# Optimization experiments

Hardware: AMD Instinct MI355X
Metric: run time of the kernel (lower is better)

Reference implementation:

```python
import jax, jax.numpy as jnp
import numpy as np

EPS = 1e-5  # torch LayerNorm default
B, P, E, H = 16, 2048, 768, 256


def setup_inputs() -> dict:
    key = jax.random.key(0)
    k_x, k_qkv, k_lw = jax.random.split(key, 3)
    return {
        "x": jax.random.normal(k_x, (B, P, E), dtype=jnp.float32),
        "norm_w": jnp.ones((P, E), dtype=jnp.float32),
        "norm_b": jnp.zeros((P, E), dtype=jnp.float32),
        "qkv_w": jax.random.normal(k_qkv, (E, 3 * H), dtype=jnp.float32) * 0.02,
        "lin_w": jax.random.normal(k_lw, (E, H), dtype=jnp.float32) * 0.02,
        "lin_b": jnp.zeros((E,), dtype=jnp.float32),
    }


def reference(x, norm_w, norm_b, qkv_w, lin_w, lin_b):
    # LayerNorm over the last TWO dims (P, E) jointly, per batch element
    mean = jnp.mean(x, axis=(1, 2), keepdims=True)
    var = jnp.var(x, axis=(1, 2), keepdims=True)
    xn = (x - mean) * jax.lax.rsqrt(var + EPS) * norm_w + norm_b

    # QKV projection: [B,P,E] @ [E,3H] -> [B,P,3H]
    qkv = jnp.einsum("bpe,eh->bph", xn, qkv_w)
    q, k, v = jnp.split(qkv, 3, axis=2)  # each [B,P,H]

    # Unnormalized attention (no scale, no softmax)
    atten = jnp.einsum("bpd,bqd->bpq", q, k)  # [B,P,P]
    o = jnp.einsum("bpq,bqd->bpd", atten, v)  # [B,P,H]

    # Dropout p=0.0 (eval) -> identity; then Linear(H -> E) + ReLU
    out = jnp.einsum("bph,eh->bpe", o, lin_w) + lin_b
    return jax.nn.relu(out)
```

## Files before the change

kernel.cpp:

```cpp
#include <hip/hip_runtime.h>
#include <cstdint>

typedef unsigned short u16;
typedef __bf16 bf16x8 __attribute__((ext_vector_type(8)));
typedef float floatx4 __attribute__((ext_vector_type(4)));

#define BB 16
#define PP 2048
#define EE 768
#define HH 256
#define PE (PP * EE)
#define MM (BB * PP)

__device__ __forceinline__ u16 f2bf(float f) {
  union { float f; uint32_t u; } v; v.f = f;
  return (u16)((v.u + 0x7fffu + ((v.u >> 16) & 1u)) >> 16);
}

__device__ __forceinline__ void gload16(const void* g, void* l) {
  typedef __attribute__((address_space(1))) const void GV;
  typedef __attribute__((address_space(3))) void LV;
  __builtin_amdgcn_global_load_lds((GV*)g, (LV*)l, 16, 0, 0);
}

__device__ __forceinline__ int xcd_remap(int orig, int nwg) {
  return (orig & 7) * (nwg >> 3) + (orig >> 3);
}

__device__ __forceinline__ void zero_acc(floatx4 acc[4][4]) {
  const floatx4 z = {0.f, 0.f, 0.f, 0.f};
#pragma unroll
  for (int i = 0; i < 4; ++i)
#pragma unroll
    for (int j = 0; j < 4; ++j) acc[i][j] = z;
}

__device__ __forceinline__ void gemm_core(const u16* A, int lda, const u16* B, int ldb,
                                          int kIters, u16* As, u16* Bs,
                                          floatx4 acc[4][4]) {
  const int tid  = threadIdx.x;
  const int lane = tid & 63;
  const int wr   = (tid >> 7) & 1;
  const int wc   = (tid >> 6) & 1;
  const int srow = tid >> 3;
  const int scol = (tid & 7) << 3;
  const int mrow = lane & 15;
  const int kgrp = (lane >> 4) << 3;
  for (int kk = 0; kk < kIters; ++kk) {
    const u16* Ak = A + kk * 64;
    const u16* Bk = B + kk * 64;
    __syncthreads();
#pragma unroll
    for (int r = 0; r < 4; ++r) {
      gload16(Ak + (size_t)(r * 32 + srow) * lda + scol, (char*)As + r * 4096 + tid * 16);
      gload16(Bk + (size_t)(r * 32 + srow) * ldb + scol, (char*)Bs + r * 4096 + tid * 16);
    }
    __syncthreads();
#pragma unroll
    for (int kp = 0; kp < 2; ++kp) {
      const int ko = kp * 32 + kgrp;
      bf16x8 af[4], bq[4];
#pragma unroll
      for (int i = 0; i < 4; ++i) {
        af[i] = *(const bf16x8*)(As + (wr * 64 + i * 16 + mrow) * 64 + ko);
        bq[i] = *(const bf16x8*)(Bs + (wc * 64 + i * 16 + mrow) * 64 + ko);
      }
#pragma unroll
      for (int i = 0; i < 4; ++i)
#pragma unroll
        for (int j = 0; j < 4; ++j)
          acc[i][j] = __builtin_amdgcn_mfma_f32_16x16x32_bf16(af[i], bq[j], acc[i][j], 0, 0, 0);
    }
  }
}

template <typename F>
__device__ __forceinline__ void epilogue(floatx4 acc[4][4], F f) {
  const int lane = threadIdx.x & 63;
  const int wr = (threadIdx.x >> 7) & 1, wc = (threadIdx.x >> 6) & 1;
  const int r0 = (lane >> 4) * 4, c0 = lane & 15;
#pragma unroll
  for (int i = 0; i < 4; ++i)
#pragma unroll
    for (int j = 0; j < 4; ++j)
#pragma unroll
      for (int r = 0; r < 4; ++r)
        f(wr * 64 + i * 16 + r0 + r, wc * 64 + j * 16 + c0, acc[i][j][r]);
}

__global__ __launch_bounds__(256) void k_reduce1(const float* __restrict__ x,
                                                 float* __restrict__ psum,
                                                 float* __restrict__ psq) {
  const int b = blockIdx.y, blk = blockIdx.x, tid = threadIdx.x;
  const float4* xb = (const float4*)(x + (size_t)b * PE + (size_t)blk * 12288);
  float s = 0.f, q = 0.f;
#pragma unroll
  for (int i = 0; i < 12; ++i) {
    float4 v = xb[tid + i * 256];
    s += v.x + v.y + v.z + v.w;
    q += v.x * v.x + v.y * v.y + v.z * v.z + v.w * v.w;
  }
  for (int off = 32; off > 0; off >>= 1) { s += __shfl_down(s, off); q += __shfl_down(q, off); }
  __shared__ float ls[4], lq[4];
  if ((tid & 63) == 0) { ls[tid >> 6] = s; lq[tid >> 6] = q; }
  __syncthreads();
  if (tid == 0) {
    psum[b * 128 + blk] = ls[0] + ls[1] + ls[2] + ls[3];
    psq [b * 128 + blk] = lq[0] + lq[1] + lq[2] + lq[3];
  }
}

__global__ void k_reduce2(const float* __restrict__ psum, const float* __restrict__ psq,
                          float* __restrict__ stats) {
  const int b = blockIdx.x, tid = threadIdx.x;
  float s = psum[b * 128 + tid], q = psq[b * 128 + tid];
  for (int off = 32; off > 0; off >>= 1) { s += __shfl_down(s, off); q += __shfl_down(q, off); }
  __shared__ float ls[2], lq[2];
  if ((tid & 63) == 0) { ls[tid >> 6] = s; lq[tid >> 6] = q; }
  __syncthreads();
  if (tid == 0) {
    float S = ls[0] + ls[1], Q = lq[0] + lq[1];
    const float invN = 1.f / (float)PE;
    float mean = S * invN;
    float var = Q * invN - mean * mean;
    stats[b * 2] = mean;
    stats[b * 2 + 1] = rsqrtf(var + 1e-5f);
  }
}

__global__ __launch_bounds__(256) void k_ln(const float* __restrict__ x,
                                            const float* __restrict__ w,
                                            const float* __restrict__ bia,
                                            const float* __restrict__ stats,
                                            u16* __restrict__ xn) {
  const float4* x4 = (const float4*)x;
  const float4* w4 = (const float4*)w;
  const float4* b4 = (const float4*)bia;
  for (int vi = blockIdx.x * 256 + threadIdx.x; vi < (PE / 4) * BB; vi += gridDim.x * 256) {
    int bidx = vi / (PE / 4);
    int wi = vi - bidx * (PE / 4);
    float4 xv = x4[vi], wv = w4[wi], bv = b4[wi];
    float mean = stats[bidx * 2], rstd = stats[bidx * 2 + 1];
    ushort4 o;
    o.x = f2bf((xv.x - mean) * rstd * wv.x + bv.x);
    o.y = f2bf((xv.y - mean) * rstd * wv.y + bv.y);
    o.z = f2bf((xv.z - mean) * rstd * wv.z + bv.z);
    o.w = f2bf((xv.w - mean) * rstd * wv.w + bv.w);
    ((ushort4*)xn)[vi] = o;
  }
}

__global__ void k_transpose_w(const float* __restrict__ src, u16* __restrict__ dst) {
  __shared__ float t[32][33];
  const int e0 = blockIdx.x * 32, n0 = blockIdx.y * 32;
  const int tx = threadIdx.x, ty = threadIdx.y;
#pragma unroll
  for (int j = 0; j < 4; ++j)
    t[ty + j * 8][tx] = src[(size_t)(e0 + ty + j * 8) * 768 + n0 + tx];
  __syncthreads();
#pragma unroll
  for (int j = 0; j < 4; ++j)
    dst[(size_t)(n0 + ty + j * 8) * 768 + e0 + tx] = f2bf(t[tx][ty + j * 8]);
}

__global__ void k_cast(const float* __restrict__ src, u16* __restrict__ dst, int n4) {
  int i = blockIdx.x * 256 + threadIdx.x;
  if (i < n4) {
    float4 v = ((const float4*)src)[i];
    ushort4 o;
    o.x = f2bf(v.x); o.y = f2bf(v.y); o.z = f2bf(v.z); o.w = f2bf(v.w);
    ((ushort4*)dst)[i] = o;
  }
}

__global__ __launch_bounds__(256) void k_gemm_qkv(const u16* __restrict__ xn,
                                                  const u16* __restrict__ wT,
                                                  u16* __restrict__ q_buf,
                                                  u16* __restrict__ kT,
                                                  u16* __restrict__ vT) {
  __shared__ __align__(16) u16 sbuf[128 * 64 * 2];
  u16* As = sbuf;
  u16* Bs = sbuf + 128 * 64;
  floatx4 acc[4][4];
  zero_acc(acc);
  const int t = xcd_remap(blockIdx.x, 1536);
  const int xt = t % 6, yt = t / 6;
  const int tM = yt * 128, tN = xt * 128;
  gemm_core(xn + (size_t)tM * EE, EE, wT + (size_t)tN * EE, EE, 12, As, Bs, acc);

  if (xt < 2) {
    epilogue(acc, [&](int gr, int gc, float v) {
      q_buf[(size_t)(tM + gr) * HH + xt * 128 + gc] = f2bf(v);
    });
  } else {
    const int b = yt >> 4;
    const int p_base = (yt & 15) * 128;
    u16* dst = ((xt < 4) ? kT : vT) + (size_t)b * (HH * PP);
    const int dbase = (xt - ((xt < 4) ? 2 : 4)) * 128;
    u16 (*tt)[144] = (u16(*)[144])sbuf;
    const int tid = threadIdx.x;
    const int lane = tid & 63;
    const int wr = (tid >> 7) & 1, wc = (tid >> 6) & 1;
    const int r0 = (lane >> 4) * 4, c0 = lane & 15;
#pragma unroll
    for (int h = 0; h < 2; ++h) {
      __syncthreads();
      if (wc == h) {
#pragma unroll
        for (int i = 0; i < 4; ++i)
#pragma unroll
          for (int j = 0; j < 4; ++j)
#pragma unroll
            for (int r = 0; r < 4; ++r)
              tt[j * 16 + c0][wr * 64 + i * 16 + r0 + r] = f2bf(acc[i][j][r]);
      }
      __syncthreads();
#pragma unroll
      for (int pass = 0; pass < 4; ++pass) {
        const int row = pass * 16 + (tid >> 4);
        const int p8 = (tid & 15) * 8;
        const int d = dbase + h * 64 + row;
        uint4 vdat = *(const uint4*)&tt[row][p8];
        *(uint4*)&dst[(size_t)d * PP + p_base + p8] = vdat;
      }
    }
  }
}

__global__ __launch_bounds__(256) void k_gemm_w2(const u16* __restrict__ kT,
                                                 const u16* __restrict__ vT,
                                                 float* __restrict__ part) {
  __shared__ __align__(16) u16 As[128 * 64], Bs[128 * 64];
  floatx4 acc[4][4];
  zero_acc(acc);
  const int t = xcd_remap(blockIdx.x, 512);
  const int xt = t & 1, yt = (t >> 1) & 1, z = t >> 2;
  const int b = z >> 3, s = z & 7;
  const int tM = yt * 128, tN = xt * 128;
  const u16* A = kT + (size_t)b * (HH * PP) + (size_t)tM * PP + s * 256;
  const u16* B = vT + (size_t)b * (HH * PP) + (size_t)tN * PP + s * 256;
  gemm_core(A, PP, B, PP, 4, As, Bs, acc);
  float* P = part + (size_t)z * 65536;
  epilogue(acc, [&](int gr, int gc, float v) {
    P[(size_t)(tM + gr) * 256 + tN + gc] = v;
  });
}

__global__ void k_reduce_w2(const float* __restrict__ part, u16* __restrict__ W2) {
  const int idx = blockIdx.x * 256 + threadIdx.x;
  const int b = idx >> 16, i = idx & 65535;
  const float* p = part + ((size_t)b << 19) + i;
  float s = 0.f;
#pragma unroll
  for (int t = 0; t < 8; ++t) s += p[(size_t)t << 16];
  W2[idx] = f2bf(s);
}

__global__ __launch_bounds__(256) void k_gemm_m2(const u16* __restrict__ lwB,
                                                 const u16* __restrict__ W2,
                                                 u16* __restrict__ M2T) {
  __shared__ __align__(16) u16 As[128 * 64], Bs[128 * 64];
  floatx4 acc[4][4];
  zero_acc(acc);
  const int t = xcd_remap(blockIdx.x, 192);
  const int xt = t & 1, yt = (t >> 1) % 6, b = t / 12;
  const int tM = yt * 128, tN = xt * 128;
  const u16* A = lwB + (size_t)tM * HH;
  const u16* B = W2 + (size_t)b * 65536 + (size_t)tN * HH;
  gemm_core(A, HH, B, HH, 4, As, Bs, acc);
  u16* Mb = M2T + (size_t)b * (EE * HH);
  epilogue(acc, [&](int gr, int gc, float v) {
    Mb[(size_t)(tM + gr) * HH + tN + gc] = f2bf(v);
  });
}

__global__ __launch_bounds__(256) void k_gemm_out(const u16* __restrict__ q_buf,
                                                  const u16* __restrict__ M2T,
                                                  const float* __restrict__ lb,
                                                  float* __restrict__ out) {
  __shared__ __align__(16) u16 As[128 * 64], Bs[128 * 64];
  floatx4 acc[4][4];
  zero_acc(acc);
  const int t = xcd_remap(blockIdx.x, 1536);
  const int xt = t % 6, yt = (t / 6) % 16, b = t / 96;
  const int tM = yt * 128, tN = xt * 128;
  const u16* A = q_buf + (size_t)b * (PP * HH) + (size_t)tM * HH;
  const u16* B = M2T + (size_t)b * (EE * HH) + (size_t)tN * HH;
  gemm_core(A, HH, B, HH, 4, As, Bs, acc);
  float* ob = out + (size_t)b * PE;
  epilogue(acc, [&](int gr, int gc, float v) {
    ob[(size_t)(tM + gr) * EE + tN + gc] = fmaxf(v + lb[tN + gc], 0.f);
  });
}

extern "C" void kernel_launch(void* const* d_in, const int* in_sizes, int n_in,
                              void* d_out, int out_size, void* d_ws, size_t ws_size,
                              hipStream_t stream) {
  (void)in_sizes; (void)n_in; (void)out_size;
  const float* x  = (const float*)d_in[0];
  const float* nw = (const float*)d_in[1];
  const float* nb = (const float*)d_in[2];
  const float* qw = (const float*)d_in[3];
  const float* lw = (const float*)d_in[4];
  const float* lb = (const float*)d_in[5];
  float* out = (float*)d_out;
  char* ws = (char*)d_ws;

  size_t off = 0;
  auto alloc = [&](size_t bytes) { size_t o = off; off += (bytes + 255) & ~(size_t)255; return o; };
  const size_t o_psum = alloc(16 * 128 * 4);
  const size_t o_psq  = alloc(16 * 128 * 4);
  const size_t o_st   = alloc(16 * 2 * 4);
  const size_t o_qwT  = alloc((size_t)768 * 768 * 2);
  const size_t o_lwB  = alloc((size_t)768 * 256 * 2);
  const size_t o_q    = alloc((size_t)MM * HH * 2);
  const size_t o_kT   = alloc((size_t)BB * HH * PP * 2);
  const size_t o_vT   = alloc((size_t)BB * HH * PP * 2);
  const size_t o_W2   = alloc((size_t)BB * HH * HH * 2);
  const size_t o_M2T  = alloc((size_t)BB * EE * HH * 2);
  const size_t need_base = off;
  const size_t region = (size_t)MM * EE * 2;

  char* big = (ws_size >= need_base + region) ? (ws + need_base) : (char*)d_out;

  float* psum = (float*)(ws + o_psum);
  float* psq  = (float*)(ws + o_psq);
  float* st   = (float*)(ws + o_st);
  u16* qwT    = (u16*)(ws + o_qwT);
  u16* lwB    = (u16*)(ws + o_lwB);
  u16* q_buf  = (u16*)(ws + o_q);
  u16* kT     = (u16*)(ws + o_kT);
  u16* vT     = (u16*)(ws + o_vT);
  u16* W2     = (u16*)(ws + o_W2);
  u16* M2T    = (u16*)(ws + o_M2T);
  u16* xn     = (u16*)big;
  float* part = (float*)big;

  k_reduce1<<<dim3(128, 16), 256, 0, stream>>>(x, psum, psq);
  k_reduce2<<<16, 128, 0, stream>>>(psum, psq, st);
  k_ln<<<2048, 256, 0, stream>>>(x, nw, nb, st, xn);
  k_transpose_w<<<dim3(24, 24), dim3(32, 8), 0, stream>>>(qw, qwT);
  k_cast<<<192, 256, 0, stream>>>(lw, lwB, 768 * 256 / 4);
  k_gemm_qkv<<<1536, 256, 0, stream>>>(xn, qwT, q_buf, kT, vT);
  k_gemm_w2<<<512, 256, 0, stream>>>(kT, vT, part);
  k_reduce_w2<<<4096, 256, 0, stream>>>(part, W2);
  k_gemm_m2<<<192, 256, 0, stream>>>(lwB, W2, M2T);
  k_gemm_out<<<1536, 256, 0, stream>>>(q_buf, M2T, lb, out);
}
```

Measured before the change: 329.7 us.

## Rewrite QKV GEMM as 256x256-tile 8-wave kernel with swizzled double-buffered LDS

Replaces the 128x128-tile QKV projection GEMM with a 256x256-tile kernel using 512 threads (8 waves), an XOR-swizzled LDS layout and double-buffered global-to-LDS loads that overlap with MFMA phases. It also adds wave priority hints. Larger tiles raise operand reuse and reduce global traffic, and the pipelining is meant to hide load latency. In exchange it uses 128KB of LDS and more accumulator registers per thread, which limits occupancy, and it launches only 384 blocks, which may leave the GPU's compute units less evenly loaded.

```diff
diff --git a/kernel.cpp b/kernel.cpp
--- a/kernel.cpp
+++ b/kernel.cpp
@@ -27,7 +27,7 @@
   return (orig & 7) * (nwg >> 3) + (orig >> 3);
 }
 
-__device__ __forceinline__ void zero_acc(floatx4 acc[4][4]) {
+__device__ __forceinline__ void zero_acc4(floatx4 acc[4][4]) {
   const floatx4 z = {0.f, 0.f, 0.f, 0.f};
 #pragma unroll
   for (int i = 0; i < 4; ++i)
@@ -75,7 +75,7 @@
 }
 
 template <typename F>
-__device__ __forceinline__ void epilogue(floatx4 acc[4][4], F f) {
+__device__ __forceinline__ void epilogue4(floatx4 acc[4][4], F f) {
   const int lane = threadIdx.x & 63;
   const int wr = (threadIdx.x >> 7) & 1, wc = (threadIdx.x >> 6) & 1;
   const int r0 = (lane >> 4) * 4, c0 = lane & 15;
@@ -86,6 +86,151 @@
 #pragma unroll
       for (int r = 0; r < 4; ++r)
         f(wr * 64 + i * 16 + r0 + r, wc * 64 + j * 16 + c0, acc[i][j][r]);
+}
+
+
+__device__ __forceinline__ void stage8(u16* sm, int bf, const u16* A, const u16* Bw,
+                                       int ks, int tid) {
+  const int colc = (((tid & 7) ^ ((tid >> 3) & 7)) << 3) + ks * 64;
+  const int rw = tid >> 3;
+#pragma unroll
+  for (int h = 0; h < 2; ++h)
+#pragma unroll
+    for (int L = 0; L < 2; ++L)
+      gload16(A + (size_t)(h * 128 + L * 64 + rw) * EE + colc,
+              (char*)sm + (size_t)(bf * 16384 + h * 8192 + L * 4096 + tid * 8) * 2);
+#pragma unroll
+  for (int h = 0; h < 2; ++h)
+#pragma unroll
+    for (int L = 0; L < 2; ++L)
+      gload16(Bw + (size_t)(h * 128 + L * 64 + rw) * EE + colc,
+              (char*)sm + (size_t)(32768 + bf * 16384 + h * 8192 + L * 4096 + tid * 8) * 2);
+}
+
+template <int IH, int JH>
+__device__ __forceinline__ void phase_mfma(const u16* sm, int bf, int wr, int wcn,
+                                           int lane, floatx4 acc[8][4]) {
+  const int m = lane & 15, hi = lane >> 4, mk = m & 7;
+  bf16x8 a[4][2], b[2][2];
+#pragma unroll
+  for (int ii = 0; ii < 4; ++ii) {
+    const int r = (IH * 4 + ii) * 16 + m;
+#pragma unroll
+    for (int kp = 0; kp < 2; ++kp)
+      a[ii][kp] = *(const bf16x8*)(sm + bf * 16384 + wr * 8192 + r * 64 +
+                                   (((kp * 4 + hi) ^ mk) << 3));
+  }
+#pragma unroll
+  for (int jj = 0; jj < 2; ++jj) {
+    const int r = (wcn & 1) * 64 + (JH * 2 + jj) * 16 + m;
+#pragma unroll
+    for (int kp = 0; kp < 2; ++kp)
+      b[jj][kp] = *(const bf16x8*)(sm + 32768 + bf * 16384 + (wcn >> 1) * 8192 + r * 64 +
+                                   (((kp * 4 + hi) ^ mk) << 3));
+  }
+  __builtin_amdgcn_s_barrier();
+  __builtin_amdgcn_s_setprio(1);
+#pragma unroll
+  for (int ii = 0; ii < 4; ++ii)
+#pragma unroll
+    for (int jj = 0; jj < 2; ++jj)
+#pragma unroll
+      for (int kp = 0; kp < 2; ++kp)
+        acc[IH * 4 + ii][JH * 2 + jj] = __builtin_amdgcn_mfma_f32_16x16x32_bf16(
+            a[ii][kp], b[jj][kp], acc[IH * 4 + ii][JH * 2 + jj], 0, 0, 0);
+  __builtin_amdgcn_s_setprio(0);
+}
+
+__global__ __launch_bounds__(512, 2) void k_gemm_qkv8(const u16* __restrict__ xn,
+                                                      const u16* __restrict__ wT,
+                                                      u16* __restrict__ q_buf,
+                                                      u16* __restrict__ kT,
+                                                      u16* __restrict__ vT) {
+  __shared__ __align__(16) u16 sm[65536];
+  floatx4 acc[8][4];
+  const floatx4 z = {0.f, 0.f, 0.f, 0.f};
+#pragma unroll
+  for (int i = 0; i < 8; ++i)
+#pragma unroll
+    for (int j = 0; j < 4; ++j) acc[i][j] = z;
+
+  const int t = xcd_remap(blockIdx.x, 384);
+  const int xt = t % 3;
+  const int yt = t / 3;
+  const int tM = yt * 256, tN = xt * 256;
+  const u16* A  = xn + (size_t)tM * EE;
+  const u16* Bw = wT + (size_t)tN * EE;
+  const int tid = threadIdx.x, lane = tid & 63, wid = tid >> 6;
+  const int wr = wid >> 2, wcn = wid & 3;
+
+  stage8(sm, 0, A, Bw, 0, tid);
+  asm volatile("s_waitcnt vmcnt(0)" ::: "memory");
+  __builtin_amdgcn_sched_barrier(0);
+  __builtin_amdgcn_s_barrier();
+
+  const int NT2 = (EE / 64) / 2;
+  for (int it = 0; it < NT2; ++it) {
+    stage8(sm, 1, A, Bw, 2 * it + 1, tid);
+    phase_mfma<0, 0>(sm, 0, wr, wcn, lane, acc);
+    __builtin_amdgcn_s_barrier();
+    phase_mfma<0, 1>(sm, 0, wr, wcn, lane, acc);
+    __builtin_amdgcn_s_barrier();
+    phase_mfma<1, 0>(sm, 0, wr, wcn, lane, acc);
+    __builtin_amdgcn_s_barrier();
+    phase_mfma<1, 1>(sm, 0, wr, wcn, lane, acc);
+    asm volatile("s_waitcnt vmcnt(0)" ::: "memory");
+    __builtin_amdgcn_sched_barrier(0);
+    __builtin_amdgcn_s_barrier();
+    if (2 * it + 2 < EE / 64) stage8(sm, 0, A, Bw, 2 * it + 2, tid);
+    phase_mfma<0, 0>(sm, 1, wr, wcn, lane, acc);
+    __builtin_amdgcn_s_barrier();
+    phase_mfma<0, 1>(sm, 1, wr, wcn, lane, acc);
+    __builtin_amdgcn_s_barrier();
+    phase_mfma<1, 0>(sm, 1, wr, wcn, lane, acc);
+    __builtin_amdgcn_s_barrier();
+    phase_mfma<1, 1>(sm, 1, wr, wcn, lane, acc);
+    asm volatile("s_waitcnt vmcnt(0)" ::: "memory");
+    __builtin_amdgcn_sched_barrier(0);
+    __builtin_amdgcn_s_barrier();
+  }
+
+  const int c0 = lane & 15, r0v = (lane >> 4) * 4;
+  if (xt == 0) {
+#pragma unroll
+    for (int i = 0; i < 8; ++i)
+#pragma unroll
+      for (int j = 0; j < 4; ++j)
+#pragma unroll
+        for (int r = 0; r < 4; ++r)
+          q_buf[(size_t)(tM + wr * 128 + i * 16 + r0v + r) * HH + wcn * 64 + j * 16 + c0] =
+              f2bf(acc[i][j][r]);
+  } else {
+    u16* dst = (xt == 1 ? kT : vT);
+    const int b = yt >> 3, p0 = (yt & 7) * 256;
+    u16* db = dst + (size_t)b * (HH * PP);
+    u16* tt = sm + wid * 8192;
+#pragma unroll
+    for (int jh = 0; jh < 2; ++jh) {
+#pragma unroll
+      for (int jj = 0; jj < 2; ++jj)
+#pragma unroll
+        for (int i = 0; i < 8; ++i) {
+          ushort4 w4;
+          w4.x = f2bf(acc[i][jh * 2 + jj][0]);
+          w4.y = f2bf(acc[i][jh * 2 + jj][1]);
+          w4.z = f2bf(acc[i][jh * 2 + jj][2]);
+          w4.w = f2bf(acc[i][jh * 2 + jj][3]);
+          *(ushort4*)&tt[(jj * 16 + c0) * 136 + i * 16 + r0v] = w4;
+        }
+#pragma unroll
+      for (int pass = 0; pass < 8; ++pass) {
+        const int dl = pass * 4 + (lane >> 4), p8 = (lane & 15) * 8;
+        uint4 vdat = *(const uint4*)&tt[dl * 136 + p8];
+        const int d = wcn * 64 + jh * 32 + dl;
+        *(uint4*)&db[(size_t)d * PP + p0 + wr * 128 + p8] = vdat;
+      }
+    }
+  }
 }
 
 __global__ __launch_bounds__(256) void k_reduce1(const float* __restrict__ x,
@@ -173,66 +318,12 @@
   }
 }
 
-__global__ __launch_bounds__(256) void k_gemm_qkv(const u16* __restrict__ xn,
-                                                  const u16* __restrict__ wT,
-                                                  u16* __restrict__ q_buf,
-                                                  u16* __restrict__ kT,
-                                                  u16* __restrict__ vT) {
-  __shared__ __align__(16) u16 sbuf[128 * 64 * 2];
-  u16* As = sbuf;
-  u16* Bs = sbuf + 128 * 64;
-  floatx4 acc[4][4];
-  zero_acc(acc);
-  const int t = xcd_remap(blockIdx.x, 1536);
-  const int xt = t % 6, yt = t / 6;
-  const int tM = yt * 128, tN = xt * 128;
-  gemm_core(xn + (size_t)tM * EE, EE, wT + (size_t)tN * EE, EE, 12, As, Bs, acc);
-
-  if (xt < 2) {
-    epilogue(acc, [&](int gr, int gc, float v) {
-      q_buf[(size_t)(tM + gr) * HH + xt * 128 + gc] = f2bf(v);
-    });
-  } else {
-    const int b = yt >> 4;
-    const int p_base = (yt & 15) * 128;
-    u16* dst = ((xt < 4) ? kT : vT) + (size_t)b * (HH * PP);
-    const int dbase = (xt - ((xt < 4) ? 2 : 4)) * 128;
-    u16 (*tt)[144] = (u16(*)[144])sbuf;
-    const int tid = threadIdx.x;
-    const int lane = tid & 63;
-    const int wr = (tid >> 7) & 1, wc = (tid >> 6) & 1;
-    const int r0 = (lane >> 4) * 4, c0 = lane & 15;
-#pragma unroll
-    for (int h = 0; h < 2; ++h) {
-      __syncthreads();
-      if (wc == h) {
-#pragma unroll
-        for (int i = 0; i < 4; ++i)
-#pragma unroll
-          for (int j = 0; j < 4; ++j)
-#pragma unroll
-            for (int r = 0; r < 4; ++r)
-              tt[j * 16 + c0][wr * 64 + i * 16 + r0 + r] = f2bf(acc[i][j][r]);
-      }
-      __syncthreads();
-#pragma unroll
-      for (int pass = 0; pass < 4; ++pass) {
-        const int row = pass * 16 + (tid >> 4);
-        const int p8 = (tid & 15) * 8;
-        const int d = dbase + h * 64 + row;
-        uint4 vdat = *(const uint4*)&tt[row][p8];
-        *(uint4*)&dst[(size_t)d * PP + p_base + p8] = vdat;
-      }
-    }
-  }
-}
-
 __global__ __launch_bounds__(256) void k_gemm_w2(const u16* __restrict__ kT,
                                                  const u16* __restrict__ vT,
                                                  float* __restrict__ part) {
   __shared__ __align__(16) u16 As[128 * 64], Bs[128 * 64];
   floatx4 acc[4][4];
-  zero_acc(acc);
+  zero_acc4(acc);
   const int t = xcd_remap(blockIdx.x, 512);
   const int xt = t & 1, yt = (t >> 1) & 1, z = t >> 2;
   const int b = z >> 3, s = z & 7;
@@ -241,7 +332,7 @@
   const u16* B = vT + (size_t)b * (HH * PP) + (size_t)tN * PP + s * 256;
   gemm_core(A, PP, B, PP, 4, As, Bs, acc);
   float* P = part + (size_t)z * 65536;
-  epilogue(acc, [&](int gr, int gc, float v) {
+  epilogue4(acc, [&](int gr, int gc, float v) {
     P[(size_t)(tM + gr) * 256 + tN + gc] = v;
   });
 }
@@ -261,7 +352,7 @@
                                                  u16* __restrict__ M2T) {
   __shared__ __align__(16) u16 As[128 * 64], Bs[128 * 64];
   floatx4 acc[4][4];
-  zero_acc(acc);
+  zero_acc4(acc);
   const int t = xcd_remap(blockIdx.x, 192);
   const int xt = t & 1, yt = (t >> 1) % 6, b = t / 12;
   const int tM = yt * 128, tN = xt * 128;
@@ -269,7 +360,7 @@
   const u16* B = W2 + (size_t)b * 65536 + (size_t)tN * HH;
   gemm_core(A, HH, B, HH, 4, As, Bs, acc);
   u16* Mb = M2T + (size_t)b * (EE * HH);
-  epilogue(acc, [&](int gr, int gc, float v) {
+  epilogue4(acc, [&](int gr, int gc, float v) {
     Mb[(size_t)(tM + gr) * HH + tN + gc] = f2bf(v);
   });
 }
@@ -280,7 +371,7 @@
                                                   float* __restrict__ out) {
   __shared__ __align__(16) u16 As[128 * 64], Bs[128 * 64];
   floatx4 acc[4][4];
-  zero_acc(acc);
+  zero_acc4(acc);
   const int t = xcd_remap(blockIdx.x, 1536);
   const int xt = t % 6, yt = (t / 6) % 16, b = t / 96;
   const int tM = yt * 128, tN = xt * 128;
@@ -288,7 +379,7 @@
   const u16* B = M2T + (size_t)b * (EE * HH) + (size_t)tN * HH;
   gemm_core(A, HH, B, HH, 4, As, Bs, acc);
   float* ob = out + (size_t)b * PE;
-  epilogue(acc, [&](int gr, int gc, float v) {
+  epilogue4(acc, [&](int gr, int gc, float v) {
     ob[(size_t)(tM + gr) * EE + tN + gc] = fmaxf(v + lb[tN + gc], 0.f);
   });
 }
@@ -341,7 +432,7 @@
   k_ln<<<2048, 256, 0, stream>>>(x, nw, nb, st, xn);
   k_transpose_w<<<dim3(24, 24), dim3(32, 8), 0, stream>>>(qw, qwT);
   k_cast<<<192, 256, 0, stream>>>(lw, lwB, 768 * 256 / 4);
-  k_gemm_qkv<<<1536, 256, 0, stream>>>(xn, qwT, q_buf, kT, vT);
+  k_gemm_qkv8<<<384, 512, 0, stream>>>(xn, qwT, q_buf, kT, vT);
   k_gemm_w2<<<512, 256, 0, stream>>>(kT, vT, part);
   k_reduce_w2<<<4096, 256, 0, stream>>>(part, W2);
   k_gemm_m2<<<192, 256, 0, stream>>>(lwB, W2, M2T);
```

After: 328.1 us. No clear change (-0.5%).

## Fuse GEMM chain into one persistent cooperative kernel with grid syncs

Applied to the files above, without the earlier changes.

Replaces the five separate GEMM/reduce launches with a single persistent cooperative kernel that steps through the phases, separated by grid-wide syncs. The weight transpose and cast kernels are merged into one prep launch. The goal is to cut per-launch overhead and tail gaps between dependent kernels. In exchange, the host runs occupancy and attribute queries on every call, and phases with fewer tiles (192, 512) leave the persistent grid partly idle.

```diff
diff --git a/kernel.cpp b/kernel.cpp
--- a/kernel.cpp
+++ b/kernel.cpp
@@ -1,5 +1,8 @@
 #include <hip/hip_runtime.h>
+#include <hip/hip_cooperative_groups.h>
 #include <cstdint>
+
+namespace cg = cooperative_groups;
 
 typedef unsigned short u16;
 typedef __bf16 bf16x8 __attribute__((ext_vector_type(8)));
@@ -27,7 +30,7 @@
   return (orig & 7) * (nwg >> 3) + (orig >> 3);
 }
 
-__device__ __forceinline__ void zero_acc(floatx4 acc[4][4]) {
+__device__ __forceinline__ void zero_acc4(floatx4 acc[4][4]) {
   const floatx4 z = {0.f, 0.f, 0.f, 0.f};
 #pragma unroll
   for (int i = 0; i < 4; ++i)
@@ -75,7 +78,7 @@
 }
 
 template <typename F>
-__device__ __forceinline__ void epilogue(floatx4 acc[4][4], F f) {
+__device__ __forceinline__ void epilogue4(floatx4 acc[4][4], F f) {
   const int lane = threadIdx.x & 63;
   const int wr = (threadIdx.x >> 7) & 1, wc = (threadIdx.x >> 6) & 1;
   const int r0 = (lane >> 4) * 4, c0 = lane & 15;
@@ -86,6 +89,189 @@
 #pragma unroll
       for (int r = 0; r < 4; ++r)
         f(wr * 64 + i * 16 + r0 + r, wc * 64 + j * 16 + c0, acc[i][j][r]);
+}
+
+
+__device__ __forceinline__ void phase_qkv(int t, const u16* __restrict__ xn,
+                                          const u16* __restrict__ wT,
+                                          u16* __restrict__ q_buf,
+                                          u16* __restrict__ kT,
+                                          u16* __restrict__ vT,
+                                          u16* As, u16* Bs) {
+  floatx4 acc[4][4];
+  zero_acc4(acc);
+  const int xt = t % 6, yt = t / 6;
+  const int tM = yt * 128, tN = xt * 128;
+  gemm_core(xn + (size_t)tM * EE, EE, wT + (size_t)tN * EE, EE, 12, As, Bs, acc);
+
+  if (xt < 2) {
+    epilogue4(acc, [&](int gr, int gc, float v) {
+      q_buf[(size_t)(tM + gr) * HH + xt * 128 + gc] = f2bf(v);
+    });
+  } else {
+    const int b = yt >> 4;
+    const int p_base = (yt & 15) * 128;
+    u16* dst = ((xt < 4) ? kT : vT) + (size_t)b * (HH * PP);
+    const int dbase = (xt - ((xt < 4) ? 2 : 4)) * 128;
+    u16 (*tp)[144] = (u16(*)[144])As;
+    const int tid = threadIdx.x;
+    const int lane = tid & 63;
+    const int wr = (tid >> 7) & 1, wc = (tid >> 6) & 1;
+    const int r0 = (lane >> 4) * 4, c0 = lane & 15;
+#pragma unroll
+    for (int h = 0; h < 2; ++h) {
+      __syncthreads();
+      if (wc == h) {
+#pragma unroll
+        for (int i = 0; i < 4; ++i)
+#pragma unroll
+          for (int j = 0; j < 4; ++j)
+#pragma unroll
+            for (int r = 0; r < 4; ++r)
+              tp[j * 16 + c0][wr * 64 + i * 16 + r0 + r] = f2bf(acc[i][j][r]);
+      }
+      __syncthreads();
+#pragma unroll
+      for (int pass = 0; pass < 4; ++pass) {
+        const int row = pass * 16 + (tid >> 4);
+        const int p8 = (tid & 15) * 8;
+        const int d = dbase + h * 64 + row;
+        uint4 vdat = *(const uint4*)&tp[row][p8];
+        *(uint4*)&dst[(size_t)d * PP + p_base + p8] = vdat;
+      }
+    }
+  }
+}
+
+__device__ __forceinline__ void phase_w2(int t, const u16* __restrict__ kT,
+                                         const u16* __restrict__ vT,
+                                         float* __restrict__ part,
+                                         u16* As, u16* Bs) {
+  floatx4 acc[4][4];
+  zero_acc4(acc);
+  const int xt = t & 1, yt = (t >> 1) & 1, z = t >> 2;
+  const int b = z >> 3, s = z & 7;
+  const int tM = yt * 128, tN = xt * 128;
+  const u16* A = kT + (size_t)b * (HH * PP) + (size_t)tM * PP + s * 256;
+  const u16* B = vT + (size_t)b * (HH * PP) + (size_t)tN * PP + s * 256;
+  gemm_core(A, PP, B, PP, 4, As, Bs, acc);
+  float* P = part + (size_t)z * 65536;
+  epilogue4(acc, [&](int gr, int gc, float v) {
+    P[(size_t)(tM + gr) * 256 + tN + gc] = v;
+  });
+}
+
+__device__ __forceinline__ void phase_rw2(int idx, const float* __restrict__ part,
+                                          u16* __restrict__ W2) {
+  const int b = idx >> 16, i = idx & 65535;
+  const float* p = part + ((size_t)b << 19) + i;
+  float s = 0.f;
+#pragma unroll
+  for (int t = 0; t < 8; ++t) s += p[(size_t)t << 16];
+  W2[idx] = f2bf(s);
+}
+
+__device__ __forceinline__ void phase_m2(int t, const u16* __restrict__ lwB,
+                                         const u16* __restrict__ W2,
+                                         u16* __restrict__ M2T,
+                                         u16* As, u16* Bs) {
+  floatx4 acc[4][4];
+  zero_acc4(acc);
+  const int xt = t & 1, yt = (t >> 1) % 6, b = t / 12;
+  const int tM = yt * 128, tN = xt * 128;
+  const u16* A = lwB + (size_t)tM * HH;
+  const u16* B = W2 + (size_t)b * 65536 + (size_t)tN * HH;
+  gemm_core(A, HH, B, HH, 4, As, Bs, acc);
+  u16* Mb = M2T + (size_t)b * (EE * HH);
+  epilogue4(acc, [&](int gr, int gc, float v) {
+    Mb[(size_t)(tM + gr) * HH + tN + gc] = f2bf(v);
+  });
+}
+
+__device__ __forceinline__ void phase_out(int t, const u16* __restrict__ q_buf,
+                                          const u16* __restrict__ M2T,
+                                          const float* __restrict__ lb,
+                                          float* __restrict__ out,
+                                          u16* As, u16* Bs) {
+  floatx4 acc[4][4];
+  zero_acc4(acc);
+  const int xt = t % 6, yt = (t / 6) % 16, b = t / 96;
+  const int tM = yt * 128, tN = xt * 128;
+  const u16* A = q_buf + (size_t)b * (PP * HH) + (size_t)tM * HH;
+  const u16* B = M2T + (size_t)b * (EE * HH) + (size_t)tN * HH;
+  gemm_core(A, HH, B, HH, 4, As, Bs, acc);
+  float* ob = out + (size_t)b * PE;
+  epilogue4(acc, [&](int gr, int gc, float v) {
+    ob[(size_t)(tM + gr) * EE + tN + gc] = fmaxf(v + lb[tN + gc], 0.f);
+  });
+}
+
+__global__ __launch_bounds__(256, 2) void k_coop(const u16* __restrict__ xn,
+                                                 const u16* __restrict__ qwT,
+                                                 u16* __restrict__ q_buf,
+                                                 u16* __restrict__ kT,
+                                                 u16* __restrict__ vT,
+                                                 float* __restrict__ part,
+                                                 u16* __restrict__ W2,
+                                                 const u16* __restrict__ lwB,
+                                                 u16* __restrict__ M2T,
+                                                 const float* __restrict__ lb,
+                                                 float* __restrict__ out) {
+  __shared__ __align__(16) u16 sbuf[128 * 64 * 2];
+  u16* As = sbuf;
+  u16* Bs = sbuf + 128 * 64;
+  cg::grid_group g = cg::this_grid();
+  const int nb = gridDim.x, bid = blockIdx.x;
+
+  for (int tt = bid; tt < 1536; tt += nb)
+    phase_qkv(xcd_remap(tt, 1536), xn, qwT, q_buf, kT, vT, As, Bs);
+  g.sync();
+  for (int tt = bid; tt < 512; tt += nb)
+    phase_w2(xcd_remap(tt, 512), kT, vT, part, As, Bs);
+  g.sync();
+  for (int idx = bid * 256 + (int)threadIdx.x; idx < (BB << 16); idx += nb * 256)
+    phase_rw2(idx, part, W2);
+  g.sync();
+  for (int tt = bid; tt < 192; tt += nb)
+    phase_m2(xcd_remap(tt, 192), lwB, W2, M2T, As, Bs);
+  g.sync();
+  for (int tt = bid; tt < 1536; tt += nb)
+    phase_out(xcd_remap(tt, 1536), q_buf, M2T, lb, out, As, Bs);
+}
+
+__global__ __launch_bounds__(256) void k_gemm_qkv(const u16* __restrict__ xn,
+                                                  const u16* __restrict__ wT,
+                                                  u16* __restrict__ q_buf,
+                                                  u16* __restrict__ kT,
+                                                  u16* __restrict__ vT) {
+  __shared__ __align__(16) u16 sbuf[128 * 64 * 2];
+  phase_qkv(xcd_remap(blockIdx.x, 1536), xn, wT, q_buf, kT, vT, sbuf, sbuf + 128 * 64);
+}
+
+__global__ __launch_bounds__(256) void k_gemm_w2(const u16* __restrict__ kT,
+                                                 const u16* __restrict__ vT,
+                                                 float* __restrict__ part) {
+  __shared__ __align__(16) u16 sbuf[128 * 64 * 2];
+  phase_w2(xcd_remap(blockIdx.x, 512), kT, vT, part, sbuf, sbuf + 128 * 64);
+}
+
+__global__ void k_reduce_w2(const float* __restrict__ part, u16* __restrict__ W2) {
+  phase_rw2(blockIdx.x * 256 + threadIdx.x, part, W2);
+}
+
+__global__ __launch_bounds__(256) void k_gemm_m2(const u16* __restrict__ lwB,
+                                                 const u16* __restrict__ W2,
+                                                 u16* __restrict__ M2T) {
+  __shared__ __align__(16) u16 sbuf[128 * 64 * 2];
+  phase_m2(xcd_remap(blockIdx.x, 192), lwB, W2, M2T, sbuf, sbuf + 128 * 64);
+}
+
+__global__ __launch_bounds__(256) void k_gemm_out(const u16* __restrict__ q_buf,
+                                                  const u16* __restrict__ M2T,
+                                                  const float* __restrict__ lb,
+                                                  float* __restrict__ out) {
+  __shared__ __align__(16) u16 sbuf[128 * 64 * 2];
+  phase_out(xcd_remap(blockIdx.x, 1536), q_buf, M2T, lb, out, sbuf, sbuf + 128 * 64);
 }
 
 __global__ __launch_bounds__(256) void k_reduce1(const float* __restrict__ x,
@@ -150,147 +336,31 @@
   }
 }
 
-__global__ void k_transpose_w(const float* __restrict__ src, u16* __restrict__ dst) {
-  __shared__ float t[32][33];
-  const int e0 = blockIdx.x * 32, n0 = blockIdx.y * 32;
-  const int tx = threadIdx.x, ty = threadIdx.y;
-#pragma unroll
-  for (int j = 0; j < 4; ++j)
-    t[ty + j * 8][tx] = src[(size_t)(e0 + ty + j * 8) * 768 + n0 + tx];
-  __syncthreads();
-#pragma unroll
-  for (int j = 0; j < 4; ++j)
-    dst[(size_t)(n0 + ty + j * 8) * 768 + e0 + tx] = f2bf(t[tx][ty + j * 8]);
-}
-
-__global__ void k_cast(const float* __restrict__ src, u16* __restrict__ dst, int n4) {
-  int i = blockIdx.x * 256 + threadIdx.x;
-  if (i < n4) {
-    float4 v = ((const float4*)src)[i];
-    ushort4 o;
-    o.x = f2bf(v.x); o.y = f2bf(v.y); o.z = f2bf(v.z); o.w = f2bf(v.w);
-    ((ushort4*)dst)[i] = o;
-  }
-}
-
-__global__ __launch_bounds__(256) void k_gemm_qkv(const u16* __restrict__ xn,
-                                                  const u16* __restrict__ wT,
-                                                  u16* __restrict__ q_buf,
-                                                  u16* __restrict__ kT,
-                                                  u16* __restrict__ vT) {
-  __shared__ __align__(16) u16 sbuf[128 * 64 * 2];
-  u16* As = sbuf;
-  u16* Bs = sbuf + 128 * 64;
-  floatx4 acc[4][4];
-  zero_acc(acc);
-  const int t = xcd_remap(blockIdx.x, 1536);
-  const int xt = t % 6, yt = t / 6;
-  const int tM = yt * 128, tN = xt * 128;
-  gemm_core(xn + (size_t)tM * EE, EE, wT + (size_t)tN * EE, EE, 12, As, Bs, acc);
-
-  if (xt < 2) {
-    epilogue(acc, [&](int gr, int gc, float v) {
-      q_buf[(size_t)(tM + gr) * HH + xt * 128 + gc] = f2bf(v);
-    });
+__global__ __launch_bounds__(256) void k_prep(const float* __restrict__ qw,
+                                              u16* __restrict__ qwT,
+                                              const float* __restrict__ lw,
+                                              u16* __restrict__ lwB) {
+  if (blockIdx.x < 576) {
+    __shared__ float tsh[32][33];
+    const int bx = blockIdx.x % 24, by = blockIdx.x / 24;
+    const int e0 = bx * 32, n0 = by * 32;
+    const int tx = threadIdx.x & 31, ty = threadIdx.x >> 5;
+#pragma unroll
+    for (int j = 0; j < 4; ++j)
+      tsh[ty + j * 8][tx] = qw[(size_t)(e0 + ty + j * 8) * 768 + n0 + tx];
+    __syncthreads();
+#pragma unroll
+    for (int j = 0; j < 4; ++j)
+      qwT[(size_t)(n0 + ty + j * 8) * 768 + e0 + tx] = f2bf(tsh[tx][ty + j * 8]);
   } else {
-    const int b = yt >> 4;
-    const int p_base = (yt & 15) * 128;
-    u16* dst = ((xt < 4) ? kT : vT) + (size_t)b * (HH * PP);
-    const int dbase = (xt - ((xt < 4) ? 2 : 4)) * 128;
-    u16 (*tt)[144] = (u16(*)[144])sbuf;
-    const int tid = threadIdx.x;
-    const int lane = tid & 63;
-    const int wr = (tid >> 7) & 1, wc = (tid >> 6) & 1;
-    const int r0 = (lane >> 4) * 4, c0 = lane & 15;
-#pragma unroll
-    for (int h = 0; h < 2; ++h) {
-      __syncthreads();
-      if (wc == h) {
-#pragma unroll
-        for (int i = 0; i < 4; ++i)
-#pragma unroll
-          for (int j = 0; j < 4; ++j)
-#pragma unroll
-            for (int r = 0; r < 4; ++r)
-              tt[j * 16 + c0][wr * 64 + i * 16 + r0 + r] = f2bf(acc[i][j][r]);
-      }
-      __syncthreads();
-#pragma unroll
-      for (int pass = 0; pass < 4; ++pass) {
-        const int row = pass * 16 + (tid >> 4);
-        const int p8 = (tid & 15) * 8;
-        const int d = dbase + h * 64 + row;
-        uint4 vdat = *(const uint4*)&tt[row][p8];
-        *(uint4*)&dst[(size_t)d * PP + p_base + p8] = vdat;
-      }
+    const int i = (blockIdx.x - 576) * 256 + threadIdx.x;
+    if (i < 768 * 256 / 4) {
+      float4 v = ((const float4*)lw)[i];
+      ushort4 o;
+      o.x = f2bf(v.x); o.y = f2bf(v.y); o.z = f2bf(v.z); o.w = f2bf(v.w);
+      ((ushort4*)lwB)[i] = o;
     }
   }
-}
-
-__global__ __launch_bounds__(256) void k_gemm_w2(const u16* __restrict__ kT,
-                                                 const u16* __restrict__ vT,
-                                                 float* __restrict__ part) {
-  __shared__ __align__(16) u16 As[128 * 64], Bs[128 * 64];
-  floatx4 acc[4][4];
-  zero_acc(acc);
-  const int t = xcd_remap(blockIdx.x, 512);
-  const int xt = t & 1, yt = (t >> 1) & 1, z = t >> 2;
-  const int b = z >> 3, s = z & 7;
-  const int tM = yt * 128, tN = xt * 128;
-  const u16* A = kT + (size_t)b * (HH * PP) + (size_t)tM * PP + s * 256;
-  const u16* B = vT + (size_t)b * (HH * PP) + (size_t)tN * PP + s * 256;
-  gemm_core(A, PP, B, PP, 4, As, Bs, acc);
-  float* P = part + (size_t)z * 65536;
-  epilogue(acc, [&](int gr, int gc, float v) {
-    P[(size_t)(tM + gr) * 256 + tN + gc] = v;
-  });
-}
-
-__global__ void k_reduce_w2(const float* __restrict__ part, u16* __restrict__ W2) {
-  const int idx = blockIdx.x * 256 + threadIdx.x;
-  const int b = idx >> 16, i = idx & 65535;
-  const float* p = part + ((size_t)b << 19) + i;
-  float s = 0.f;
-#pragma unroll
-  for (int t = 0; t < 8; ++t) s += p[(size_t)t << 16];
-  W2[idx] = f2bf(s);
-}
-
-__global__ __launch_bounds__(256) void k_gemm_m2(const u16* __restrict__ lwB,
-                                                 const u16* __restrict__ W2,
-                                                 u16* __restrict__ M2T) {
-  __shared__ __align__(16) u16 As[128 * 64], Bs[128 * 64];
-  floatx4 acc[4][4];
-  zero_acc(acc);
-  const int t = xcd_remap(blockIdx.x, 192);
-  const int xt = t & 1, yt = (t >> 1) % 6, b = t / 12;
-  const int tM = yt * 128, tN = xt * 128;
-  const u16* A = lwB + (size_t)tM * HH;
-  const u16* B = W2 + (size_t)b * 65536 + (size_t)tN * HH;
-  gemm_core(A, HH, B, HH, 4, As, Bs, acc);
-  u16* Mb = M2T + (size_t)b * (EE * HH);
-  epilogue(acc, [&](int gr, int gc, float v) {
-    Mb[(size_t)(tM + gr) * HH + tN + gc] = f2bf(v);
-  });
-}
-
-__global__ __launch_bounds__(256) void k_gemm_out(const u16* __restrict__ q_buf,
-                                                  const u16* __restrict__ M2T,
-                                                  const float* __restrict__ lb,
-                                                  float* __restrict__ out) {
-  __shared__ __align__(16) u16 As[128 * 64], Bs[128 * 64];
-  floatx4 acc[4][4];
-  zero_acc(acc);
-  const int t = xcd_remap(blockIdx.x, 1536);
-  const int xt = t % 6, yt = (t / 6) % 16, b = t / 96;
-  const int tM = yt * 128, tN = xt * 128;
-  const u16* A = q_buf + (size_t)b * (PP * HH) + (size_t)tM * HH;
-  const u16* B = M2T + (size_t)b * (EE * HH) + (size_t)tN * HH;
-  gemm_core(A, HH, B, HH, 4, As, Bs, acc);
-  float* ob = out + (size_t)b * PE;
-  epilogue(acc, [&](int gr, int gc, float v) {
-    ob[(size_t)(tM + gr) * EE + tN + gc] = fmaxf(v + lb[tN + gc], 0.f);
-  });
 }
 
 extern "C" void kernel_launch(void* const* d_in, const int* in_sizes, int n_in,
@@ -333,17 +403,37 @@
   u16* vT     = (u16*)(ws + o_vT);
   u16* W2     = (u16*)(ws + o_W2);
   u16* M2T    = (u16*)(ws + o_M2T);
-  u16* xn     = (u16*)big;
+  const u16* xn = (const u16*)big;
+  u16* xn_w   = (u16*)big;
   float* part = (float*)big;
 
   k_reduce1<<<dim3(128, 16), 256, 0, stream>>>(x, psum, psq);
   k_reduce2<<<16, 128, 0, stream>>>(psum, psq, st);
-  k_ln<<<2048, 256, 0, stream>>>(x, nw, nb, st, xn);
-  k_transpose_w<<<dim3(24, 24), dim3(32, 8), 0, stream>>>(qw, qwT);
-  k_cast<<<192, 256, 0, stream>>>(lw, lwB, 768 * 256 / 4);
-  k_gemm_qkv<<<1536, 256, 0, stream>>>(xn, qwT, q_buf, kT, vT);
-  k_gemm_w2<<<512, 256, 0, stream>>>(kT, vT, part);
-  k_reduce_w2<<<4096, 256, 0, stream>>>(part, W2);
-  k_gemm_m2<<<192, 256, 0, stream>>>(lwB, W2, M2T);
-  k_gemm_out<<<1536, 256, 0, stream>>>(q_buf, M2T, lb, out);
-}
+  k_ln<<<2048, 256, 0, stream>>>(x, nw, nb, st, xn_w);
+  k_prep<<<768, 256, 0, stream>>>(qw, qwT, lw, lwB);
+
+  int dev = 0;
+  hipGetDevice(&dev);
+  int coop = 0;
+  hipDeviceGetAttribute(&coop, hipDeviceAttributeCooperativeLaunch, dev);
+  int maxb = 0;
+  hipOccupancyMaxActiveBlocksPerMultiprocessor(&maxb, k_coop, 256, 0);
+  int grid = maxb * 256;
+  if (grid > 1536) grid = 1536;
+
+  bool done = false;
+  if (coop && grid >= 256) {
+    void* args[] = {(void*)&xn, (void*)&qwT, (void*)&q_buf, (void*)&kT, (void*)&vT,
+                    (void*)&part, (void*)&W2, (void*)&lwB, (void*)&M2T, (void*)&lb,
+                    (void*)&out};
+    hipError_t e = hipLaunchCooperativeKernel(k_coop, dim3(grid), dim3(256), args, 0, stream);
+    done = (e == hipSuccess);
+  }
+  if (!done) {
+    k_gemm_qkv<<<1536, 256, 0, stream>>>(xn, qwT, q_buf, kT, vT);
+    k_gemm_w2<<<512, 256, 0, stream>>>(kT, vT, part);
+    k_reduce_w2<<<4096, 256, 0, stream>>>(part, W2);
+    k_gemm_m2<<<192, 256, 0, stream>>>(lwB, W2, M2T);
+    k_gemm_out<<<1536, 256, 0, stream>>>(q_buf, M2T, lb, out);
+  }
+}
```

New measurement: 534.7 us. 1.62x slower.
